# Kernel tuning notes

Measured on AMD Instinct MI355X. Metric: run time of the kernel, lower is better.

## Reference

```python
import jax, jax.numpy as jnp
import numpy as np

B, S, HID, NH = 8, 384, 512, 8
HD = HID // NH
SCALE = float(np.sqrt(HID))  # torch code scales by sqrt(full hidden_units), not head dim
EPS = 1e-6


def setup_inputs() -> dict:
    key = jax.random.key(0)
    ks = jax.random.split(key, 6)
    enc = jax.random.normal(ks[0], (B, S, HID), jnp.float32)
    # mask: (B,1,S,S); fill=ones, made causal (lower-triangular) so masking is exercised
    mask = jnp.broadcast_to(jnp.tril(jnp.ones((S, S), jnp.int32)), (B, 1, S, S))
    init = 1.0 / np.sqrt(HID)
    Wq = jax.random.normal(ks[1], (HID, HID), jnp.float32) * init
    Wk = jax.random.normal(ks[2], (HID, HID), jnp.float32) * init
    Wv = jax.random.normal(ks[3], (HID, HID), jnp.float32) * init
    Wo = jax.random.normal(ks[4], (HID, HID), jnp.float32) * init
    ln_gamma = jnp.ones((HID,), jnp.float32)
    ln_beta = jnp.zeros((HID,), jnp.float32)
    return {"enc": enc, "mask": mask, "Wq": Wq, "Wk": Wk, "Wv": Wv, "Wo": Wo,
            "ln_gamma": ln_gamma, "ln_beta": ln_beta}


def reference(enc, mask, Wq, Wk, Wv, Wo, ln_gamma, ln_beta):
    # enc: (B,S,HID); torch Linear(no bias): y = x @ W.T
    def heads(x, W):
        return (x @ W.T).reshape(B, S, NH, HD).transpose(0, 2, 1, 3)  # (B,H,S,D)

    q, k, v = heads(enc, Wq), heads(enc, Wk), heads(enc, Wv)
    # intersample scores: query (b,h,q) vs key (c,h,k) -> (B,H,C,Sq,Sk)
    scores = jnp.einsum('bhqd,chkd->bhcqk', q, k) / SCALE
    m = mask[:, 0]  # (C,S,S): key-sample mask
    scores = jnp.where(m[None, None] == 0, -1.0e9, scores)
    # joint softmax over (key-sample c, key-position k)
    sw = scores.transpose(0, 1, 3, 2, 4).reshape(B, NH, S, B * S)
    w = jax.nn.softmax(sw, axis=-1).reshape(B, NH, S, B, S).transpose(0, 1, 3, 2, 4)  # (B,H,C,Sq,Sk)
    ctx = jnp.einsum('bhcqk,chkd->bhqd', w, v)            # (B,H,S,D)
    ctx = ctx.transpose(0, 2, 1, 3).reshape(B, S, HID)     # (B,S,HID)
    out = ctx @ Wo.T + enc                                 # W_O + residual (dropout=identity, eval)
    mu = out.mean(-1, keepdims=True)
    var = ((out - mu) ** 2).mean(-1, keepdims=True)
    out = (out - mu) / jnp.sqrt(var + EPS) * ln_gamma + ln_beta
    return (out, w)
```

## Files before the change

### kernel.cpp

```cpp
#include <hip/hip_runtime.h>
#include <hip/hip_cooperative_groups.h>
#include <hip/hip_bf16.h>

namespace cg = cooperative_groups;

#define B_    8
#define S_    384
#define HID_  512
#define NH_   8
#define HD_   64
#define T_    3072
static constexpr float INV_SCALE = 0.044194173824159216f;

typedef float  f32x4  __attribute__((ext_vector_type(4)));
typedef __bf16 bf16x8 __attribute__((ext_vector_type(8)));
typedef __bf16 bf16x4 __attribute__((ext_vector_type(4)));

#define MFMA(a, b, c) __builtin_amdgcn_mfma_f32_16x16x32_bf16((a), (b), (c), 0, 0, 0)

#define NBLK 256
#define NTHR 512


__device__ __forceinline__ void cvt_unit(int i,
    const float* __restrict__ enc, const float* __restrict__ Wq,
    const float* __restrict__ Wk,  const float* __restrict__ Wv,
    const float* __restrict__ Wo,
    __bf16* __restrict__ encB, __bf16* __restrict__ WqB,
    __bf16* __restrict__ WkB,  __bf16* __restrict__ WvB,
    __bf16* __restrict__ WoB)
{
    const int E  = T_ * HID_ / 4;
    const int W4 = HID_ * HID_ / 4;
    const float* src; __bf16* dst; int off;
    if      (i < E)          { src = enc; dst = encB; off = i; }
    else if (i < E + W4)     { src = Wq;  dst = WqB;  off = i - E; }
    else if (i < E + 2 * W4) { src = Wk;  dst = WkB;  off = i - E - W4; }
    else if (i < E + 3 * W4) { src = Wv;  dst = WvB;  off = i - E - 2 * W4; }
    else                     { src = Wo;  dst = WoB;  off = i - E - 3 * W4; }
    f32x4 v = *(const f32x4*)(src + (size_t)off * 4);
    bf16x4 o;
    #pragma unroll
    for (int j = 0; j < 4; ++j) o[j] = (__bf16)v[j];
    *(bf16x4*)(dst + (size_t)off * 4) = o;
}

__device__ __forceinline__ void qkv_unit(int vb, int t2,
    const __bf16* __restrict__ encB, const __bf16* __restrict__ WqB,
    const __bf16* __restrict__ WkB,  const __bf16* __restrict__ WvB,
    __bf16* __restrict__ Qs, __bf16* __restrict__ Ks, __bf16* __restrict__ Vt)
{
    const int w    = t2 >> 6;
    const int lane = t2 & 63;
    const int col  = lane & 15;
    const int quad = lane >> 4;
    const int x  = vb % 48;
    const int y  = (vb / 48) % 8;
    const int z  = vb / 384;
    const int m0 = x * 64 + w * 16;
    const int n0 = y * 64;
    const __bf16* W = (z == 0) ? WqB : (z == 1) ? WkB : WvB;

    f32x4 acc[4];
    #pragma unroll
    for (int j = 0; j < 4; ++j) acc[j] = (f32x4){0.f, 0.f, 0.f, 0.f};

    const __bf16* arow = encB + (size_t)(m0 + col) * HID_;
    for (int k0 = 0; k0 < HID_; k0 += 32) {
        bf16x8 a = *(const bf16x8*)(arow + k0 + quad * 8);
        #pragma unroll
        for (int j = 0; j < 4; ++j) {
            bf16x8 b = *(const bf16x8*)(W + (size_t)(n0 + j * 16 + col) * HID_ + k0 + quad * 8);
            acc[j] = MFMA(a, b, acc[j]);
        }
    }

    if (z == 2) {
        #pragma unroll
        for (int j = 0; j < 4; ++j) {
            int n = n0 + j * 16 + col;
            bf16x4 pk;
            #pragma unroll
            for (int r = 0; r < 4; ++r) pk[r] = (__bf16)acc[j][r];
            *(bf16x4*)(Vt + (size_t)n * T_ + m0 + quad * 4) = pk;
        }
    } else {
        __bf16* Oo = (z == 0) ? Qs : Ks;
        float sc = (z == 0) ? INV_SCALE : 1.0f;
        #pragma unroll
        for (int j = 0; j < 4; ++j)
            #pragma unroll
            for (int r = 0; r < 4; ++r)
                Oo[(size_t)(m0 + quad * 4 + r) * HID_ + n0 + j * 16 + col] =
                    (__bf16)(acc[j][r] * sc);
    }
}

__device__ __forceinline__ void attn_unit(int u, int tid, char* smem,
    const __bf16* __restrict__ Qs, const __bf16* __restrict__ Ks,
    const __bf16* __restrict__ Vt, __bf16* __restrict__ ctxB,
    float* __restrict__ rlws, __bf16* __restrict__ eB,
    float* __restrict__ wout, int useBf16)
{
    const int qt   = u % 6;
    const int h    = (u / 6) % 8;
    const int b    = u / 48;
    const int W    = tid >> 6;
    const int half = W >> 2;
    const int w    = W & 3;
    const int lane = tid & 63;
    const int col  = lane & 15;
    const int quad = lane >> 4;

    __bf16 (*elds)[16][72] = (__bf16(*)[16][72])(smem);
    float  (*cred)[16][68] = (float(*)[16][68])(smem + 18432);
    float  (*lred)[16][16] = (float(*)[16][16])(smem + 35840);

    const int qq_base = w * 16 + quad * 4;

    const __bf16* qrow = Qs + (size_t)(b * S_ + qt * 64 + w * 16 + col) * HID_ + h * HD_;
    bf16x8 aQ0 = *(const bf16x8*)(qrow + quad * 8);
    bf16x8 aQ1 = *(const bf16x8*)(qrow + 32 + quad * 8);

    f32x4 acc[4];
    #pragma unroll
    for (int j = 0; j < 4; ++j) acc[j] = (f32x4){0.f, 0.f, 0.f, 0.f};
    float lp[4] = {0.f, 0.f, 0.f, 0.f};

    const size_t qg   = (size_t)(b * NH_ + h) * S_ + qt * 64 + w * 16 + col;
    __bf16* ebase = eB + qg * T_;
    float*  wbase = wout + (((size_t)(b * NH_ + h) * B_) * S_ + qt * 64 + w * 16 + col) * S_;

    const int NC = B_ * (qt + 1);
    for (int idx = half; idx < NC; idx += 2) {
        const int c  = idx / (qt + 1);
        const int kc = idx % (qt + 1);
        const int kt0 = c * S_ + kc * 64;
        const bool diag = (kc == qt);
        #pragma unroll
        for (int nt = 0; nt < 4; ++nt) {
            const __bf16* krow = Ks + (size_t)(kt0 + nt * 16 + col) * HID_ + h * HD_;
            bf16x8 bK0 = *(const bf16x8*)(krow + quad * 8);
            bf16x8 bK1 = *(const bf16x8*)(krow + 32 + quad * 8);
            f32x4 s = (f32x4){0.f, 0.f, 0.f, 0.f};
            s = MFMA(aQ0, bK0, s);
            s = MFMA(aQ1, bK1, s);
            const int kk = nt * 16 + col;
            #pragma unroll
            for (int r = 0; r < 4; ++r) {
                float e = (!diag || kk <= qq_base + r) ? __expf(s[r]) : 0.f;
                lp[r] += e;
                elds[W][quad * 4 + r][kk] = (__bf16)e;
            }
        }
        #pragma unroll
        for (int ks = 0; ks < 2; ++ks) {
            bf16x8 aE = *(const bf16x8*)(&elds[W][col][ks * 32 + quad * 8]);
            if (useBf16) {
                *(bf16x8*)(ebase + c * S_ + kc * 64 + ks * 32 + quad * 8) = aE;
            } else {
                float* wp = wbase + (size_t)c * S_ * S_ + kc * 64 + ks * 32 + quad * 8;
                f32x4 lo, hi;
                #pragma unroll
                for (int j = 0; j < 4; ++j) { lo[j] = (float)aE[j]; hi[j] = (float)aE[j + 4]; }
                *(f32x4*)wp = lo;
                *(f32x4*)(wp + 4) = hi;
            }
            #pragma unroll
            for (int nt = 0; nt < 4; ++nt) {
                bf16x8 bV = *(const bf16x8*)(Vt + (size_t)(h * HD_ + nt * 16 + col) * T_ +
                                             kt0 + ks * 32 + quad * 8);
                acc[nt] = MFMA(aE, bV, acc[nt]);
            }
        }
    }

    if (half == 1) {
        #pragma unroll
        for (int nt = 0; nt < 4; ++nt)
            #pragma unroll
            for (int r = 0; r < 4; ++r)
                cred[w][quad * 4 + r][nt * 16 + col] = acc[nt][r];
        #pragma unroll
        for (int r = 0; r < 4; ++r)
            lred[w][quad * 4 + r][col] = lp[r];
    }
    __syncthreads();
    if (half == 0) {
        #pragma unroll
        for (int r = 0; r < 4; ++r)
            lp[r] += lred[w][quad * 4 + r][col];
        #pragma unroll
        for (int nt = 0; nt < 4; ++nt)
            #pragma unroll
            for (int r = 0; r < 4; ++r)
                acc[nt][r] += cred[w][quad * 4 + r][nt * 16 + col];

        float rl[4];
        #pragma unroll
        for (int r = 0; r < 4; ++r) {
            float v = lp[r];
            v += __shfl_xor(v, 1);
            v += __shfl_xor(v, 2);
            v += __shfl_xor(v, 4);
            v += __shfl_xor(v, 8);
            rl[r] = 1.0f / v;
        }
        if (col == 0) {
            #pragma unroll
            for (int r = 0; r < 4; ++r)
                rlws[(size_t)(b * NH_ + h) * S_ + qt * 64 + qq_base + r] = rl[r];
        }
        #pragma unroll
        for (int nt = 0; nt < 4; ++nt)
            #pragma unroll
            for (int r = 0; r < 4; ++r)
                ctxB[(size_t)(b * S_ + qt * 64 + qq_base + r) * HID_ + h * HD_ + nt * 16 + col] =
                    (__bf16)(acc[nt][r] * rl[r]);
    }
}

__global__ __launch_bounds__(512, 2)
void mega1(const float* __restrict__ enc,
           const float* __restrict__ Wq,  const float* __restrict__ Wk,
           const float* __restrict__ Wv,  const float* __restrict__ Wo,
           __bf16* __restrict__ encB, __bf16* __restrict__ WqB,
           __bf16* __restrict__ WkB,  __bf16* __restrict__ WvB,
           __bf16* __restrict__ WoB,
           __bf16* __restrict__ Qs,   __bf16* __restrict__ Ks,
           __bf16* __restrict__ Vt,   __bf16* __restrict__ ctxB,
           float* __restrict__ rlws,  __bf16* __restrict__ eB,
           float* __restrict__ wout,  int useBf16)
{
    cg::grid_group grid = cg::this_grid();
    const int blk = blockIdx.x;
    const int tid = threadIdx.x;

    __shared__ __align__(16) char smem[39936];

    {
        const int TOT = T_ * HID_ / 4 + HID_ * HID_;
        for (int i = blk * NTHR + tid; i < TOT; i += NBLK * NTHR)
            cvt_unit(i, enc, Wq, Wk, Wv, Wo, encB, WqB, WkB, WvB, WoB);
    }
    grid.sync();

    {
        const int half = tid >> 8;
        const int t2   = tid & 255;
        for (int u = blk; u < 576; u += NBLK)
            qkv_unit(u * 2 + half, t2, encB, WqB, WkB, WvB, Qs, Ks, Vt);
    }
    grid.sync();

    for (int u = blk; u < 384; u += NBLK) {
        attn_unit(u, tid, smem, Qs, Ks, Vt, ctxB, rlws, eB, wout, useBf16);
        __syncthreads();
    }
}

__global__ __launch_bounds__(256)
void cvt_kernel(const float* enc, const float* Wq, const float* Wk,
                const float* Wv, const float* Wo,
                __bf16* encB, __bf16* WqB, __bf16* WkB, __bf16* WvB, __bf16* WoB)
{
    int i = blockIdx.x * 256 + threadIdx.x;
    cvt_unit(i, enc, Wq, Wk, Wv, Wo, encB, WqB, WkB, WvB, WoB);
}

__global__ __launch_bounds__(256)
void qkv_kernel(const __bf16* encB, const __bf16* WqB, const __bf16* WkB,
                const __bf16* WvB, __bf16* Qs, __bf16* Ks, __bf16* Vt)
{
    int vb = blockIdx.x + 48 * (blockIdx.y + 8 * blockIdx.z);
    qkv_unit(vb, threadIdx.x, encB, WqB, WkB, WvB, Qs, Ks, Vt);
}

__global__ __launch_bounds__(512)
void attn_sep(const __bf16* Qs, const __bf16* Ks, const __bf16* Vt,
              __bf16* ctxB, float* rlws, __bf16* eB, float* wout, int useBf16)
{
    __shared__ __align__(16) char smem[39936];
    attn_unit(blockIdx.x, threadIdx.x, smem, Qs, Ks, Vt, ctxB, rlws, eB, wout, useBf16);
}

__global__ __launch_bounds__(256)
void tail2(const float* __restrict__ rlws, const __bf16* __restrict__ eB,
           const __bf16* __restrict__ ctxB, const __bf16* __restrict__ WoB,
           const float* __restrict__ enc, const float* __restrict__ gamma,
           const float* __restrict__ beta, float* __restrict__ wout,
           float* __restrict__ out, int useBf16)
{
    const int tid = threadIdx.x;

    if (blockIdx.x < 192) {
        const int w    = tid >> 6;
        const int lane = tid & 63;
        const int col  = lane & 15;
        const int quad = lane >> 4;
        __shared__ float s_sums[16][4][2];

        const int t0 = blockIdx.x * 16;
        const int wv = w;

        f32x4 acc[8];
        #pragma unroll
        for (int nt = 0; nt < 8; ++nt) acc[nt] = (f32x4){0.f, 0.f, 0.f, 0.f};

        const __bf16* arow = ctxB + (size_t)(t0 + col) * HID_;
        for (int step = 0; step < 16; ++step) {
            bf16x8 a = *(const bf16x8*)(arow + step * 32 + quad * 8);
            #pragma unroll
            for (int nt = 0; nt < 8; ++nt) {
                bf16x8 bW = *(const bf16x8*)(WoB + (size_t)(wv * 128 + nt * 16 + col) * HID_ +
                                             step * 32 + quad * 8);
                acc[nt] = MFMA(a, bW, acc[nt]);
            }
        }

        const int trow = t0 + quad * 4;
        float psum[4] = {0.f, 0.f, 0.f, 0.f};
        float psq[4]  = {0.f, 0.f, 0.f, 0.f};
        #pragma unroll
        for (int nt = 0; nt < 8; ++nt) {
            int n = wv * 128 + nt * 16 + col;
            #pragma unroll
            for (int r = 0; r < 4; ++r) {
                float x = acc[nt][r] + enc[(size_t)(trow + r) * HID_ + n];
                acc[nt][r] = x;
                psum[r] += x;
                psq[r]  += x * x;
            }
        }
        #pragma unroll
        for (int r = 0; r < 4; ++r) {
            float v = psum[r], q2 = psq[r];
            v  += __shfl_xor(v, 1);  v  += __shfl_xor(v, 2);
            v  += __shfl_xor(v, 4);  v  += __shfl_xor(v, 8);
            q2 += __shfl_xor(q2, 1); q2 += __shfl_xor(q2, 2);
            q2 += __shfl_xor(q2, 4); q2 += __shfl_xor(q2, 8);
            if (col == 0) {
                s_sums[quad * 4 + r][wv][0] = v;
                s_sums[quad * 4 + r][wv][1] = q2;
            }
        }
        __syncthreads();

        #pragma unroll
        for (int r = 0; r < 4; ++r) {
            float sm = s_sums[quad * 4 + r][0][0] + s_sums[quad * 4 + r][1][0] +
                       s_sums[quad * 4 + r][2][0] + s_sums[quad * 4 + r][3][0];
            float sq = s_sums[quad * 4 + r][0][1] + s_sums[quad * 4 + r][1][1] +
                       s_sums[quad * 4 + r][2][1] + s_sums[quad * 4 + r][3][1];
            float mu   = sm * (1.0f / 512.0f);
            float var  = sq * (1.0f / 512.0f) - mu * mu;
            float rstd = rsqrtf(var + 1e-6f);
            #pragma unroll
            for (int nt = 0; nt < 8; ++nt) {
                int n = wv * 128 + nt * 16 + col;
                float y = (acc[nt][r] - mu) * rstd * gamma[n] + beta[n];
                out[(size_t)(trow + r) * HID_ + n] = y;
            }
        }
        return;
    }

    const int u  = blockIdx.x - 192;
    const int bh = u >> 3;
    const int c  = u & 7;
    float* wbase = wout + ((size_t)bh * B_ + c) * S_ * S_;
    const __bf16* ebase = eB + (size_t)bh * S_ * T_ + c * S_;
    const float* rlbase = rlws + (size_t)bh * S_;

    const int NCHUNK = S_ * (S_ / 8);
    for (int idx = tid; idx < NCHUNK; idx += 256) {
        const int q  = idx / 48;
        const int k8 = (idx - q * 48) * 8;
        float* wp = wbase + (size_t)q * S_ + k8;
        if ((k8 >> 6) > (q >> 6)) {
            *(f32x4*)wp       = (f32x4){0.f, 0.f, 0.f, 0.f};
            *(f32x4*)(wp + 4) = (f32x4){0.f, 0.f, 0.f, 0.f};
        } else {
            const float rl = rlbase[q];
            f32x4 lo, hi;
            if (useBf16) {
                bf16x8 e = *(const bf16x8*)(ebase + (size_t)q * T_ + k8);
                #pragma unroll
                for (int j = 0; j < 4; ++j) { lo[j] = (float)e[j] * rl; hi[j] = (float)e[j + 4] * rl; }
            } else {
                f32x4 e0 = *(const f32x4*)wp;
                f32x4 e1 = *(const f32x4*)(wp + 4);
                #pragma unroll
                for (int j = 0; j < 4; ++j) { lo[j] = e0[j] * rl; hi[j] = e1[j] * rl; }
            }
            *(f32x4*)wp       = lo;
            *(f32x4*)(wp + 4) = hi;
        }
    }
}

extern "C" void kernel_launch(void* const* d_in, const int* in_sizes, int n_in,
                              void* d_out, int out_size, void* d_ws, size_t ws_size,
                              hipStream_t stream)
{
    const float* enc   = (const float*)d_in[0];
    const float* Wq    = (const float*)d_in[2];
    const float* Wk    = (const float*)d_in[3];
    const float* Wv    = (const float*)d_in[4];
    const float* Wo    = (const float*)d_in[5];
    const float* gamma = (const float*)d_in[6];
    const float* beta  = (const float*)d_in[7];

    float* out  = (float*)d_out;
    float* wout = out + (size_t)T_ * HID_;

    char* ws = (char*)d_ws;
    const size_t SZ_TOK = (size_t)T_ * HID_ * sizeof(__bf16);
    const size_t SZ_W   = (size_t)HID_ * HID_ * sizeof(__bf16);
    __bf16* encB = (__bf16*)(ws);
    __bf16* WqB  = (__bf16*)(ws + SZ_TOK);
    __bf16* WkB  = (__bf16*)(ws + SZ_TOK + SZ_W);
    __bf16* WvB  = (__bf16*)(ws + SZ_TOK + 2 * SZ_W);
    __bf16* WoB  = (__bf16*)(ws + SZ_TOK + 3 * SZ_W);
    __bf16* Qs   = (__bf16*)(ws + SZ_TOK + 4 * SZ_W);
    __bf16* Ks   = (__bf16*)(ws + 2 * SZ_TOK + 4 * SZ_W);
    __bf16* Vt   = (__bf16*)(ws + 3 * SZ_TOK + 4 * SZ_W);
    __bf16* ctxB = (__bf16*)(ws + 4 * SZ_TOK + 4 * SZ_W);
    float*  rlws = (float*)(ws);

    const size_t BASE   = 5 * SZ_TOK + 4 * SZ_W;
    const size_t SZ_EB  = (size_t)(B_ * NH_) * S_ * T_ * sizeof(__bf16);
    int useBf16 = (ws_size >= BASE + SZ_EB) ? 1 : 0;
    __bf16* eB = (__bf16*)(ws + BASE);

    static int coop_ok = -1;
    if (coop_ok < 0) {
        int dev = 0;
        (void)hipGetDevice(&dev);
        int attr = 0;
        (void)hipDeviceGetAttribute(&attr, hipDeviceAttributeCooperativeLaunch, dev);
        int occ = 0;
        (void)hipOccupancyMaxActiveBlocksPerMultiprocessor(&occ, mega1, NTHR, 0);
        int nCU = 0;
        (void)hipDeviceGetAttribute(&nCU, hipDeviceAttributeMultiprocessorCount, dev);
        coop_ok = (attr != 0 && occ >= 1 && (long)occ * nCU >= NBLK) ? 1 : 0;
    }

    bool done = false;
    if (coop_ok == 1) {
        void* args[] = {
            (void*)&enc, (void*)&Wq, (void*)&Wk, (void*)&Wv, (void*)&Wo,
            (void*)&encB, (void*)&WqB, (void*)&WkB, (void*)&WvB, (void*)&WoB,
            (void*)&Qs, (void*)&Ks, (void*)&Vt, (void*)&ctxB,
            (void*)&rlws, (void*)&eB, (void*)&wout, (void*)&useBf16
        };
        hipError_t e = hipLaunchCooperativeKernel((void*)mega1, dim3(NBLK),
                                                  dim3(NTHR), args, 0, stream);
        if (e == hipSuccess) done = true;
        else coop_ok = 0;
    }
    if (!done) {
        cvt_kernel<<<dim3(2560), 256, 0, stream>>>(enc, Wq, Wk, Wv, Wo,
                                                   encB, WqB, WkB, WvB, WoB);
        qkv_kernel<<<dim3(48, 8, 3), 256, 0, stream>>>(encB, WqB, WkB, WvB, Qs, Ks, Vt);
        attn_sep<<<dim3(384), 512, 0, stream>>>(Qs, Ks, Vt, ctxB, rlws, eB, wout, useBf16);
    }

    tail2<<<dim3(192 + 512), 256, 0, stream>>>(rlws, eB, ctxB, WoB, enc,
                                               gamma, beta, wout, out, useBf16);
}
```

Before: 665.7 us.

## Fold output projection and weight scaling into cooperative megakernel, size grid to occupancy

Moves the Wo projection + residual + layernorm and the softmax weight rescale into the cooperative megakernel behind a third grid sync, so the separate tail launch is dropped. The grid is now sized from occupancy × CU count (clamped 256..1024) instead of a fixed 256, and attention tiles run in reverse q-tile order so the heaviest causal tiles start first. The tail GEMM now uses 8 waves of 64 columns each. The extra grid barrier and larger grid raise synchronisation cost.

```diff
diff --git a/kernel.cpp b/kernel.cpp
--- a/kernel.cpp
+++ b/kernel.cpp
@@ -18,7 +18,6 @@
 
 #define MFMA(a, b, c) __builtin_amdgcn_mfma_f32_16x16x32_bf16((a), (b), (c), 0, 0, 0)
 
-#define NBLK 256
 #define NTHR 512
 
 
@@ -96,15 +95,12 @@
     }
 }
 
-__device__ __forceinline__ void attn_unit(int u, int tid, char* smem,
+__device__ __forceinline__ void attn_unit(int qt, int h, int b, int tid, char* smem,
     const __bf16* __restrict__ Qs, const __bf16* __restrict__ Ks,
     const __bf16* __restrict__ Vt, __bf16* __restrict__ ctxB,
     float* __restrict__ rlws, __bf16* __restrict__ eB,
     float* __restrict__ wout, int useBf16)
 {
-    const int qt   = u % 6;
-    const int h    = (u / 6) % 8;
-    const int b    = u / 48;
     const int W    = tid >> 6;
     const int half = W >> 2;
     const int w    = W & 3;
@@ -220,160 +216,18 @@
     }
 }
 
-__global__ __launch_bounds__(512, 2)
-void mega1(const float* __restrict__ enc,
-           const float* __restrict__ Wq,  const float* __restrict__ Wk,
-           const float* __restrict__ Wv,  const float* __restrict__ Wo,
-           __bf16* __restrict__ encB, __bf16* __restrict__ WqB,
-           __bf16* __restrict__ WkB,  __bf16* __restrict__ WvB,
-           __bf16* __restrict__ WoB,
-           __bf16* __restrict__ Qs,   __bf16* __restrict__ Ks,
-           __bf16* __restrict__ Vt,   __bf16* __restrict__ ctxB,
-           float* __restrict__ rlws,  __bf16* __restrict__ eB,
-           float* __restrict__ wout,  int useBf16)
-{
-    cg::grid_group grid = cg::this_grid();
-    const int blk = blockIdx.x;
-    const int tid = threadIdx.x;
-
-    __shared__ __align__(16) char smem[39936];
-
-    {
-        const int TOT = T_ * HID_ / 4 + HID_ * HID_;
-        for (int i = blk * NTHR + tid; i < TOT; i += NBLK * NTHR)
-            cvt_unit(i, enc, Wq, Wk, Wv, Wo, encB, WqB, WkB, WvB, WoB);
-    }
-    grid.sync();
-
-    {
-        const int half = tid >> 8;
-        const int t2   = tid & 255;
-        for (int u = blk; u < 576; u += NBLK)
-            qkv_unit(u * 2 + half, t2, encB, WqB, WkB, WvB, Qs, Ks, Vt);
-    }
-    grid.sync();
-
-    for (int u = blk; u < 384; u += NBLK) {
-        attn_unit(u, tid, smem, Qs, Ks, Vt, ctxB, rlws, eB, wout, useBf16);
-        __syncthreads();
-    }
-}
-
-__global__ __launch_bounds__(256)
-void cvt_kernel(const float* enc, const float* Wq, const float* Wk,
-                const float* Wv, const float* Wo,
-                __bf16* encB, __bf16* WqB, __bf16* WkB, __bf16* WvB, __bf16* WoB)
-{
-    int i = blockIdx.x * 256 + threadIdx.x;
-    cvt_unit(i, enc, Wq, Wk, Wv, Wo, encB, WqB, WkB, WvB, WoB);
-}
-
-__global__ __launch_bounds__(256)
-void qkv_kernel(const __bf16* encB, const __bf16* WqB, const __bf16* WkB,
-                const __bf16* WvB, __bf16* Qs, __bf16* Ks, __bf16* Vt)
-{
-    int vb = blockIdx.x + 48 * (blockIdx.y + 8 * blockIdx.z);
-    qkv_unit(vb, threadIdx.x, encB, WqB, WkB, WvB, Qs, Ks, Vt);
-}
-
-__global__ __launch_bounds__(512)
-void attn_sep(const __bf16* Qs, const __bf16* Ks, const __bf16* Vt,
-              __bf16* ctxB, float* rlws, __bf16* eB, float* wout, int useBf16)
-{
-    __shared__ __align__(16) char smem[39936];
-    attn_unit(blockIdx.x, threadIdx.x, smem, Qs, Ks, Vt, ctxB, rlws, eB, wout, useBf16);
-}
-
-__global__ __launch_bounds__(256)
-void tail2(const float* __restrict__ rlws, const __bf16* __restrict__ eB,
-           const __bf16* __restrict__ ctxB, const __bf16* __restrict__ WoB,
-           const float* __restrict__ enc, const float* __restrict__ gamma,
-           const float* __restrict__ beta, float* __restrict__ wout,
-           float* __restrict__ out, int useBf16)
-{
-    const int tid = threadIdx.x;
-
-    if (blockIdx.x < 192) {
-        const int w    = tid >> 6;
-        const int lane = tid & 63;
-        const int col  = lane & 15;
-        const int quad = lane >> 4;
-        __shared__ float s_sums[16][4][2];
-
-        const int t0 = blockIdx.x * 16;
-        const int wv = w;
-
-        f32x4 acc[8];
-        #pragma unroll
-        for (int nt = 0; nt < 8; ++nt) acc[nt] = (f32x4){0.f, 0.f, 0.f, 0.f};
-
-        const __bf16* arow = ctxB + (size_t)(t0 + col) * HID_;
-        for (int step = 0; step < 16; ++step) {
-            bf16x8 a = *(const bf16x8*)(arow + step * 32 + quad * 8);
-            #pragma unroll
-            for (int nt = 0; nt < 8; ++nt) {
-                bf16x8 bW = *(const bf16x8*)(WoB + (size_t)(wv * 128 + nt * 16 + col) * HID_ +
-                                             step * 32 + quad * 8);
-                acc[nt] = MFMA(a, bW, acc[nt]);
-            }
-        }
-
-        const int trow = t0 + quad * 4;
-        float psum[4] = {0.f, 0.f, 0.f, 0.f};
-        float psq[4]  = {0.f, 0.f, 0.f, 0.f};
-        #pragma unroll
-        for (int nt = 0; nt < 8; ++nt) {
-            int n = wv * 128 + nt * 16 + col;
-            #pragma unroll
-            for (int r = 0; r < 4; ++r) {
-                float x = acc[nt][r] + enc[(size_t)(trow + r) * HID_ + n];
-                acc[nt][r] = x;
-                psum[r] += x;
-                psq[r]  += x * x;
-            }
-        }
-        #pragma unroll
-        for (int r = 0; r < 4; ++r) {
-            float v = psum[r], q2 = psq[r];
-            v  += __shfl_xor(v, 1);  v  += __shfl_xor(v, 2);
-            v  += __shfl_xor(v, 4);  v  += __shfl_xor(v, 8);
-            q2 += __shfl_xor(q2, 1); q2 += __shfl_xor(q2, 2);
-            q2 += __shfl_xor(q2, 4); q2 += __shfl_xor(q2, 8);
-            if (col == 0) {
-                s_sums[quad * 4 + r][wv][0] = v;
-                s_sums[quad * 4 + r][wv][1] = q2;
-            }
-        }
-        __syncthreads();
-
-        #pragma unroll
-        for (int r = 0; r < 4; ++r) {
-            float sm = s_sums[quad * 4 + r][0][0] + s_sums[quad * 4 + r][1][0] +
-                       s_sums[quad * 4 + r][2][0] + s_sums[quad * 4 + r][3][0];
-            float sq = s_sums[quad * 4 + r][0][1] + s_sums[quad * 4 + r][1][1] +
-                       s_sums[quad * 4 + r][2][1] + s_sums[quad * 4 + r][3][1];
-            float mu   = sm * (1.0f / 512.0f);
-            float var  = sq * (1.0f / 512.0f) - mu * mu;
-            float rstd = rsqrtf(var + 1e-6f);
-            #pragma unroll
-            for (int nt = 0; nt < 8; ++nt) {
-                int n = wv * 128 + nt * 16 + col;
-                float y = (acc[nt][r] - mu) * rstd * gamma[n] + beta[n];
-                out[(size_t)(trow + r) * HID_ + n] = y;
-            }
-        }
-        return;
-    }
-
-    const int u  = blockIdx.x - 192;
-    const int bh = u >> 3;
-    const int c  = u & 7;
+__device__ __forceinline__ void wscale_unit(int u2, int tid, int nthr,
+    const float* __restrict__ rlws, const __bf16* __restrict__ eB,
+    float* __restrict__ wout, int useBf16)
+{
+    const int bh = u2 >> 3;
+    const int c  = u2 & 7;
     float* wbase = wout + ((size_t)bh * B_ + c) * S_ * S_;
     const __bf16* ebase = eB + (size_t)bh * S_ * T_ + c * S_;
     const float* rlbase = rlws + (size_t)bh * S_;
 
     const int NCHUNK = S_ * (S_ / 8);
-    for (int idx = tid; idx < NCHUNK; idx += 256) {
+    for (int idx = tid; idx < NCHUNK; idx += nthr) {
         const int q  = idx / 48;
         const int k8 = (idx - q * 48) * 8;
         float* wp = wbase + (size_t)q * S_ + k8;
@@ -397,6 +251,238 @@
             *(f32x4*)(wp + 4) = hi;
         }
     }
+}
+
+__global__ __launch_bounds__(512, 2)
+void mega2(const float* __restrict__ enc,
+           const float* __restrict__ Wq,  const float* __restrict__ Wk,
+           const float* __restrict__ Wv,  const float* __restrict__ Wo,
+           const float* __restrict__ gamma, const float* __restrict__ beta,
+           __bf16* __restrict__ encB, __bf16* __restrict__ WqB,
+           __bf16* __restrict__ WkB,  __bf16* __restrict__ WvB,
+           __bf16* __restrict__ WoB,
+           __bf16* __restrict__ Qs,   __bf16* __restrict__ Ks,
+           __bf16* __restrict__ Vt,   __bf16* __restrict__ ctxB,
+           float* __restrict__ rlws,  __bf16* __restrict__ eB,
+           float* __restrict__ wout,  float* __restrict__ out, int useBf16)
+{
+    cg::grid_group grid = cg::this_grid();
+    const int blk  = blockIdx.x;
+    const int nblk = gridDim.x;
+    const int tid  = threadIdx.x;
+
+    __shared__ __align__(16) char smem[39936];
+
+    {
+        const int TOT = T_ * HID_ / 4 + HID_ * HID_;
+        for (int i = blk * NTHR + tid; i < TOT; i += nblk * NTHR)
+            cvt_unit(i, enc, Wq, Wk, Wv, Wo, encB, WqB, WkB, WvB, WoB);
+    }
+    grid.sync();
+
+    {
+        const int half = tid >> 8;
+        const int t2   = tid & 255;
+        for (int u = blk; u < 576; u += nblk)
+            qkv_unit(u * 2 + half, t2, encB, WqB, WkB, WvB, Qs, Ks, Vt);
+    }
+    grid.sync();
+
+    for (int i = blk; i < 384; i += nblk) {
+        const int qt = 5 - (i >> 6);
+        const int r  = i & 63;
+        attn_unit(qt, r & 7, r >> 3, tid, smem, Qs, Ks, Vt, ctxB, rlws, eB, wout, useBf16);
+        __syncthreads();
+    }
+    grid.sync();
+
+    for (int u = blk; u < 704; u += nblk) {
+        if (u < 192) {
+            const int t0   = u * 16;
+            const int wv   = tid >> 6;
+            const int lane = tid & 63;
+            const int col  = lane & 15;
+            const int quad = lane >> 4;
+            float (*s_sums)[8][2] = (float(*)[8][2])(smem + 34816);
+
+            f32x4 acc[4];
+            #pragma unroll
+            for (int nt = 0; nt < 4; ++nt) acc[nt] = (f32x4){0.f, 0.f, 0.f, 0.f};
+
+            const __bf16* arow = ctxB + (size_t)(t0 + col) * HID_;
+            for (int step = 0; step < 16; ++step) {
+                bf16x8 a = *(const bf16x8*)(arow + step * 32 + quad * 8);
+                #pragma unroll
+                for (int nt = 0; nt < 4; ++nt) {
+                    bf16x8 bW = *(const bf16x8*)(WoB + (size_t)(wv * 64 + nt * 16 + col) * HID_ +
+                                                 step * 32 + quad * 8);
+                    acc[nt] = MFMA(a, bW, acc[nt]);
+                }
+            }
+
+            const int trow = t0 + quad * 4;
+            float psum[4] = {0.f, 0.f, 0.f, 0.f};
+            float psq[4]  = {0.f, 0.f, 0.f, 0.f};
+            #pragma unroll
+            for (int nt = 0; nt < 4; ++nt) {
+                int n = wv * 64 + nt * 16 + col;
+                #pragma unroll
+                for (int r = 0; r < 4; ++r) {
+                    float x = acc[nt][r] + enc[(size_t)(trow + r) * HID_ + n];
+                    acc[nt][r] = x;
+                    psum[r] += x;
+                    psq[r]  += x * x;
+                }
+            }
+            #pragma unroll
+            for (int r = 0; r < 4; ++r) {
+                float v = psum[r], q2 = psq[r];
+                v  += __shfl_xor(v, 1);  v  += __shfl_xor(v, 2);
+                v  += __shfl_xor(v, 4);  v  += __shfl_xor(v, 8);
+                q2 += __shfl_xor(q2, 1); q2 += __shfl_xor(q2, 2);
+                q2 += __shfl_xor(q2, 4); q2 += __shfl_xor(q2, 8);
+                if (col == 0) {
+                    s_sums[quad * 4 + r][wv][0] = v;
+                    s_sums[quad * 4 + r][wv][1] = q2;
+                }
+            }
+            __syncthreads();
+
+            #pragma unroll
+            for (int r = 0; r < 4; ++r) {
+                float sm = 0.f, sq = 0.f;
+                #pragma unroll
+                for (int q = 0; q < 8; ++q) {
+                    sm += s_sums[quad * 4 + r][q][0];
+                    sq += s_sums[quad * 4 + r][q][1];
+                }
+                float mu   = sm * (1.0f / 512.0f);
+                float var  = sq * (1.0f / 512.0f) - mu * mu;
+                float rstd = rsqrtf(var + 1e-6f);
+                #pragma unroll
+                for (int nt = 0; nt < 4; ++nt) {
+                    int n = wv * 64 + nt * 16 + col;
+                    float y = (acc[nt][r] - mu) * rstd * gamma[n] + beta[n];
+                    out[(size_t)(trow + r) * HID_ + n] = y;
+                }
+            }
+            __syncthreads();
+        } else {
+            wscale_unit(u - 192, tid, NTHR, rlws, eB, wout, useBf16);
+        }
+    }
+}
+
+__global__ __launch_bounds__(256)
+void cvt_kernel(const float* enc, const float* Wq, const float* Wk,
+                const float* Wv, const float* Wo,
+                __bf16* encB, __bf16* WqB, __bf16* WkB, __bf16* WvB, __bf16* WoB)
+{
+    int i = blockIdx.x * 256 + threadIdx.x;
+    cvt_unit(i, enc, Wq, Wk, Wv, Wo, encB, WqB, WkB, WvB, WoB);
+}
+
+__global__ __launch_bounds__(256)
+void qkv_kernel(const __bf16* encB, const __bf16* WqB, const __bf16* WkB,
+                const __bf16* WvB, __bf16* Qs, __bf16* Ks, __bf16* Vt)
+{
+    int vb = blockIdx.x + 48 * (blockIdx.y + 8 * blockIdx.z);
+    qkv_unit(vb, threadIdx.x, encB, WqB, WkB, WvB, Qs, Ks, Vt);
+}
+
+__global__ __launch_bounds__(512)
+void attn_sep(const __bf16* Qs, const __bf16* Ks, const __bf16* Vt,
+              __bf16* ctxB, float* rlws, __bf16* eB, float* wout, int useBf16)
+{
+    __shared__ __align__(16) char smem[39936];
+    const int i  = blockIdx.x;
+    const int qt = 5 - (i >> 6);
+    const int r  = i & 63;
+    attn_unit(qt, r & 7, r >> 3, threadIdx.x, smem, Qs, Ks, Vt, ctxB, rlws, eB, wout, useBf16);
+}
+
+__global__ __launch_bounds__(256)
+void tail2(const float* __restrict__ rlws, const __bf16* __restrict__ eB,
+           const __bf16* __restrict__ ctxB, const __bf16* __restrict__ WoB,
+           const float* __restrict__ enc, const float* __restrict__ gamma,
+           const float* __restrict__ beta, float* __restrict__ wout,
+           float* __restrict__ out, int useBf16)
+{
+    const int tid = threadIdx.x;
+
+    if (blockIdx.x < 192) {
+        const int w    = tid >> 6;
+        const int lane = tid & 63;
+        const int col  = lane & 15;
+        const int quad = lane >> 4;
+        __shared__ float s_sums[16][4][2];
+
+        const int t0 = blockIdx.x * 16;
+        const int wv = w;
+
+        f32x4 acc[8];
+        #pragma unroll
+        for (int nt = 0; nt < 8; ++nt) acc[nt] = (f32x4){0.f, 0.f, 0.f, 0.f};
+
+        const __bf16* arow = ctxB + (size_t)(t0 + col) * HID_;
+        for (int step = 0; step < 16; ++step) {
+            bf16x8 a = *(const bf16x8*)(arow + step * 32 + quad * 8);
+            #pragma unroll
+            for (int nt = 0; nt < 8; ++nt) {
+                bf16x8 bW = *(const bf16x8*)(WoB + (size_t)(wv * 128 + nt * 16 + col) * HID_ +
+                                             step * 32 + quad * 8);
+                acc[nt] = MFMA(a, bW, acc[nt]);
+            }
+        }
+
+        const int trow = t0 + quad * 4;
+        float psum[4] = {0.f, 0.f, 0.f, 0.f};
+        float psq[4]  = {0.f, 0.f, 0.f, 0.f};
+        #pragma unroll
+        for (int nt = 0; nt < 8; ++nt) {
+            int n = wv * 128 + nt * 16 + col;
+            #pragma unroll
+            for (int r = 0; r < 4; ++r) {
+                float x = acc[nt][r] + enc[(size_t)(trow + r) * HID_ + n];
+                acc[nt][r] = x;
+                psum[r] += x;
+                psq[r]  += x * x;
+            }
+        }
+        #pragma unroll
+        for (int r = 0; r < 4; ++r) {
+            float v = psum[r], q2 = psq[r];
+            v  += __shfl_xor(v, 1);  v  += __shfl_xor(v, 2);
+            v  += __shfl_xor(v, 4);  v  += __shfl_xor(v, 8);
+            q2 += __shfl_xor(q2, 1); q2 += __shfl_xor(q2, 2);
+            q2 += __shfl_xor(q2, 4); q2 += __shfl_xor(q2, 8);
+            if (col == 0) {
+                s_sums[quad * 4 + r][wv][0] = v;
+                s_sums[quad * 4 + r][wv][1] = q2;
+            }
+        }
+        __syncthreads();
+
+        #pragma unroll
+        for (int r = 0; r < 4; ++r) {
+            float sm = s_sums[quad * 4 + r][0][0] + s_sums[quad * 4 + r][1][0] +
+                       s_sums[quad * 4 + r][2][0] + s_sums[quad * 4 + r][3][0];
+            float sq = s_sums[quad * 4 + r][0][1] + s_sums[quad * 4 + r][1][1] +
+                       s_sums[quad * 4 + r][2][1] + s_sums[quad * 4 + r][3][1];
+            float mu   = sm * (1.0f / 512.0f);
+            float var  = sq * (1.0f / 512.0f) - mu * mu;
+            float rstd = rsqrtf(var + 1e-6f);
+            #pragma unroll
+            for (int nt = 0; nt < 8; ++nt) {
+                int n = wv * 128 + nt * 16 + col;
+                float y = (acc[nt][r] - mu) * rstd * gamma[n] + beta[n];
+                out[(size_t)(trow + r) * HID_ + n] = y;
+            }
+        }
+        return;
+    }
+
+    wscale_unit(blockIdx.x - 192, tid, 256, rlws, eB, wout, useBf16);
 }
 
 extern "C" void kernel_launch(void* const* d_in, const int* in_sizes, int n_in,
@@ -434,28 +520,39 @@
     __bf16* eB = (__bf16*)(ws + BASE);
 
     static int coop_ok = -1;
+    static int nblk = 256;
     if (coop_ok < 0) {
         int dev = 0;
         (void)hipGetDevice(&dev);
         int attr = 0;
         (void)hipDeviceGetAttribute(&attr, hipDeviceAttributeCooperativeLaunch, dev);
         int occ = 0;
-        (void)hipOccupancyMaxActiveBlocksPerMultiprocessor(&occ, mega1, NTHR, 0);
+        (void)hipOccupancyMaxActiveBlocksPerMultiprocessor(&occ, mega2, NTHR, 0);
         int nCU = 0;
         (void)hipDeviceGetAttribute(&nCU, hipDeviceAttributeMultiprocessorCount, dev);
-        coop_ok = (attr != 0 && occ >= 1 && (long)occ * nCU >= NBLK) ? 1 : 0;
+        coop_ok = (attr != 0 && occ >= 1) ? 1 : 0;
+        long g = (long)occ * (long)nCU;
+        if (g < 256)  g = 256;
+        if (g > 1024) g = 1024;
+        nblk = (int)g;
     }
 
     bool done = false;
     if (coop_ok == 1) {
         void* args[] = {
             (void*)&enc, (void*)&Wq, (void*)&Wk, (void*)&Wv, (void*)&Wo,
+            (void*)&gamma, (void*)&beta,
             (void*)&encB, (void*)&WqB, (void*)&WkB, (void*)&WvB, (void*)&WoB,
             (void*)&Qs, (void*)&Ks, (void*)&Vt, (void*)&ctxB,
-            (void*)&rlws, (void*)&eB, (void*)&wout, (void*)&useBf16
+            (void*)&rlws, (void*)&eB, (void*)&wout, (void*)&out, (void*)&useBf16
         };
-        hipError_t e = hipLaunchCooperativeKernel((void*)mega1, dim3(NBLK),
+        hipError_t e = hipLaunchCooperativeKernel((void*)mega2, dim3(nblk),
                                                   dim3(NTHR), args, 0, stream);
+        if (e != hipSuccess && nblk > 256) {
+            nblk = 256;
+            e = hipLaunchCooperativeKernel((void*)mega2, dim3(nblk),
+                                           dim3(NTHR), args, 0, stream);
+        }
         if (e == hipSuccess) done = true;
         else coop_ok = 0;
     }
@@ -464,8 +561,7 @@
                                                    encB, WqB, WkB, WvB, WoB);
         qkv_kernel<<<dim3(48, 8, 3), 256, 0, stream>>>(encB, WqB, WkB, WvB, Qs, Ks, Vt);
         attn_sep<<<dim3(384), 512, 0, stream>>>(Qs, Ks, Vt, ctxB, rlws, eB, wout, useBf16);
-    }
-
-    tail2<<<dim3(192 + 512), 256, 0, stream>>>(rlws, eB, ctxB, WoB, enc,
-                                               gamma, beta, wout, out, useBf16);
-}
+        tail2<<<dim3(192 + 512), 256, 0, stream>>>(rlws, eB, ctxB, WoB, enc,
+                                                   gamma, beta, wout, out, useBf16);
+    }
+}
```

Result: faster. 559.3 us (-16.0%).
